# Kernel optimization log

Measured on AMD Instinct MI355X. Metric: run time of the kernel, lower is better.

Reference implementation:

```python
import jax, jax.numpy as jnp
import numpy as np

B, X, S, D_IN, D_OUT = 8, 8, 1024, 512, 64


def setup_inputs() -> dict:
    key = jax.random.key(0)
    ks = jax.random.split(key, 6)
    return {
        "inputs_for_keys": jax.random.normal(ks[0], (B, X, S, D_IN), dtype=jnp.float32),
        "inputs_for_values": jax.random.normal(ks[1], (B, X, S, D_IN), dtype=jnp.float32),
        "inputs_for_queries": jax.random.normal(ks[2], (B, X, S, D_IN), dtype=jnp.float32),
        "k_weight": jax.random.normal(ks[3], (D_IN, D_OUT), dtype=jnp.float32) * (2.0 / (D_IN + D_OUT)) ** 0.5,
        "v_weight": jax.random.normal(ks[4], (D_IN, D_OUT), dtype=jnp.float32) * (2.0 / (D_IN + D_OUT)) ** 0.5,
        "q_weight": jax.random.normal(ks[5], (D_IN, D_OUT), dtype=jnp.float32) * (2.0 / (D_IN + D_OUT)) ** 0.5,
    }


def reference(inputs_for_keys, inputs_for_values, inputs_for_queries, k_weight, v_weight, q_weight):
    # Projections: 'ixjk,kl->ixjl'
    K = jnp.einsum('bxsk,kl->bxsl', inputs_for_keys, k_weight)
    V = jnp.einsum('bxsk,kl->bxsl', inputs_for_values, v_weight)
    Q = jnp.einsum('bxsk,kl->bxsl', inputs_for_queries, q_weight)
    wk = K.shape[2]  # window_size_keys (NOTE: original scales by sqrt(seq_len), not sqrt(d_k))
    scores = jnp.einsum('bxqd,bxkd->bxqk', Q, K) / jnp.sqrt(jnp.float32(wk))
    # causal mask: triu(-inf, k=1) since is_self_attention=True
    causal = jnp.triu(jnp.ones((Q.shape[2], wk), dtype=bool), k=1)  # [Sq, Sk]
    scores = jnp.where(causal[None, None, :, :], -jnp.inf, scores)
    attn = jax.nn.softmax(scores, axis=-1)
    return jnp.einsum('bxqk,bxkd->bxqd', attn, V)
```

## Files before the change

### kernel.cpp

```cpp
#include <hip/hip_runtime.h>
#include <hip/hip_bf16.h>


typedef short  short8 __attribute__((ext_vector_type(8)));
typedef float  f32x4  __attribute__((ext_vector_type(4)));

#define DIN   512
#define DOUT  64
#define SEQ   1024
#define NROWS 65536

__device__ __forceinline__ unsigned short f2bf(float f) {
    unsigned int u = __float_as_uint(f);
    u += 0x7FFF + ((u >> 16) & 1);
    return (unsigned short)(u >> 16);
}

__device__ __forceinline__ unsigned short f2bf_rhu(float f) {
    return (unsigned short)((__float_as_uint(f) + 0x8000u) >> 16);
}

__device__ __forceinline__ float fast_exp2(float x) {
    float r;
    asm("v_exp_f32 %0, %1" : "=v"(r) : "v"(x));
    return r;
}

__global__ __launch_bounds__(256)
void wprep_kernel(const float* __restrict__ k_w, const float* __restrict__ v_w,
                  const float* __restrict__ q_w, unsigned short* __restrict__ Wfrag)
{
    const int mode = blockIdx.y;
    const float* w = (mode == 0) ? k_w : (mode == 1) ? v_w : q_w;
    const float sc = (mode == 2) ? 0.0450842200277801f : 1.0f;
    unsigned short* outp = Wfrag + (size_t)mode * 32768;

    const int s  = blockIdx.x * 256 + threadIdx.x;
    const int l  = s & 63;
    const int nt = (s >> 6) & 3;
    const int kk = s >> 8;
    const int lr = l & 15, lg = l >> 4;
    short8 frag;
    #pragma unroll
    for (int j = 0; j < 8; ++j)
        frag[j] = (short)f2bf(w[(kk * 32 + lg * 8 + j) * 64 + nt * 16 + lr] * sc);
    *(short8*)&outp[(size_t)s * 8] = frag;
}

__global__ __launch_bounds__(512, 2)
void proj_kernel(const float* __restrict__ k_in, const float* __restrict__ v_in,
                 const float* __restrict__ q_in,
                 const unsigned short* __restrict__ Wfrag,
                 unsigned short* __restrict__ Kb, unsigned short* __restrict__ Vf,
                 unsigned short* __restrict__ Qb)
{
    const int mode = blockIdx.y;
    const float* in = (mode == 0) ? k_in : (mode == 1) ? v_in : q_in;
    const unsigned short* wf = Wfrag + (size_t)mode * 32768;

    __shared__ __align__(16) unsigned short Wlds[32768];
    __shared__ __align__(16) unsigned short Alds[2][16384];

    const int tid = threadIdx.x;
    const int wid = tid >> 6;
    const int l   = tid & 63;
    const int lr  = l & 15;
    const int lg  = l >> 4;
    const int r0  = blockIdx.x * 128;

    const int srow = tid >> 5;
    const int scol = tid & 31;
    const float* sbase = in + (size_t)(r0 + srow) * DIN + scol * 4;

    f32x4 rA[8], rB[8];

    #define LOADC(r, c)                                                        \
        { _Pragma("unroll")                                                    \
          for (int i = 0; i < 8; ++i)                                          \
              r[i] = __builtin_nontemporal_load(                               \
                  (const f32x4*)(sbase + (size_t)i * 16 * DIN + (c) * 128)); }

    #define WRITEC(buf, r)                                                     \
        { _Pragma("unroll")                                                    \
          for (int i = 0; i < 8; ++i) {                                        \
              const int row = srow + i * 16;                                   \
              ushort4 pk;                                                      \
              pk.x = f2bf(r[i].x); pk.y = f2bf(r[i].y);                        \
              pk.z = f2bf(r[i].z); pk.w = f2bf(r[i].w);                        \
              *(ushort4*)((char*)&Alds[buf][0] +                               \
                  ((row * 256 + scol * 8) ^ ((row & 7) << 4))) = pk;           \
          } }

    const int arow  = wid * 16 + lr;
    const int abase = arow * 256 + lg * 16;
    const int aswz  = (arow & 7) << 4;

    f32x4 acc[4];
    #pragma unroll
    for (int nt = 0; nt < 4; ++nt)
        #pragma unroll
        for (int i = 0; i < 4; ++i) acc[nt][i] = 0.f;

    #define COMPUTEC(buf, c)                                                   \
        { _Pragma("unroll")                                                    \
          for (int k = 0; k < 4; ++k) {                                        \
              const short8 af = *(const short8*)((const char*)&Alds[buf][0] +  \
                                  ((abase + k * 64) ^ aswz));                  \
              const int kk = (c) * 4 + k;                                      \
              _Pragma("unroll")                                                \
              for (int nt = 0; nt < 4; ++nt) {                                 \
                  const short8 bf = *(const short8*)&Wlds[((kk * 4 + nt) * 64 + l) * 8]; \
                  acc[nt] = __builtin_amdgcn_mfma_f32_16x16x32_bf16(af, bf, acc[nt], 0, 0, 0); \
              }                                                                \
          } }

    LOADC(rA, 0);
    LOADC(rB, 1);
    #pragma unroll
    for (int i = 0; i < 8; ++i)
        *(short8*)&Wlds[(i * 512 + tid) * 8] = *(const short8*)&wf[(size_t)(i * 512 + tid) * 8];
    WRITEC(0, rA);
    __syncthreads();

    LOADC(rA, 2);
    WRITEC(1, rB);
    COMPUTEC(0, 0);
    __syncthreads();
    LOADC(rB, 3);
    WRITEC(0, rA);
    COMPUTEC(1, 1);
    __syncthreads();
    WRITEC(1, rB);
    COMPUTEC(0, 2);
    __syncthreads();
    COMPUTEC(1, 3);

    if (mode == 1) {
        const int grow = r0 + wid * 16 + lg * 4;
        const int bx = grow >> 10;
        const int sl = grow & 1023;
        const int sg = sl >> 5;
        const int lp = (((sl & 31) >> 3) << 4) | lr;
        const int j0 = sl & 7;
        #pragma unroll
        for (int nt = 0; nt < 4; ++nt) {
            ushort4 pk;
            pk.x = f2bf(acc[nt][0]); pk.y = f2bf(acc[nt][1]);
            pk.z = f2bf(acc[nt][2]); pk.w = f2bf(acc[nt][3]);
            *(ushort4*)&Vf[(((size_t)bx * 32 + sg) * 4 + nt) * 512 + (size_t)lp * 8 + j0] = pk;
        }
    } else {
        unsigned short* outp = (mode == 0) ? Kb : Qb;
        const int rbase = r0 + wid * 16 + lg * 4;
        #pragma unroll
        for (int nt = 0; nt < 4; ++nt)
            #pragma unroll
            for (int i = 0; i < 4; ++i)
                outp[(size_t)(rbase + i) * 64 + nt * 16 + lr] = f2bf(acc[nt][i]);
    }
    #undef LOADC
    #undef WRITEC
    #undef COMPUTEC
}

__global__ __launch_bounds__(512)
void attn_kernel(const unsigned short* __restrict__ Qb,
                 const unsigned short* __restrict__ Kb,
                 const unsigned short* __restrict__ Vf,
                 float* __restrict__ out)
{
    __shared__ __align__(16) unsigned short Plds[8][16][72];
    __shared__ __align__(16) f32x4 RedAcc[4][64][4];
    __shared__ float RedSum[4][64][4];

    const int tid  = threadIdx.x;
    const int wid  = tid >> 6;
    const int g    = wid & 3;
    const int half = wid >> 2;
    const int l    = tid & 63;
    const int lr   = l & 15;
    const int lg   = l >> 4;
    const int bx   = blockIdx.x;
    const int qblk = 15 - (int)blockIdx.y;
    const int qw0  = qblk * 64 + g * 16;

    const unsigned short* Qp = Qb + (size_t)bx * 65536;
    const unsigned short* Kp = Kb + (size_t)bx * 65536;
    const unsigned short* Vp = Vf + (size_t)bx * 65536;

    const short8 qa0 = *(const short8*)&Qp[(size_t)(qw0 + lr) * 64 + lg * 8];
    const short8 qa1 = *(const short8*)&Qp[(size_t)(qw0 + lr) * 64 + 32 + lg * 8];

    const int qrow = qw0 + lg * 4;

    float lsum[4] = {0.f, 0.f, 0.f, 0.f};
    f32x4 acc[4];
    #pragma unroll
    for (int dt = 0; dt < 4; ++dt)
        #pragma unroll
        for (int i = 0; i < 4; ++i) acc[dt][i] = 0.f;

    for (int kb = half * 64; kb <= qw0; kb += 128) {
        #pragma unroll
        for (int kt = 0; kt < 4; ++kt) {
            const int kbase = kb + kt * 16;
            if (kbase <= qw0) {
                const short8 k0 = *(const short8*)&Kp[(size_t)(kbase + lr) * 64 + lg * 8];
                const short8 k1 = *(const short8*)&Kp[(size_t)(kbase + lr) * 64 + 32 + lg * 8];
                f32x4 t;
                #pragma unroll
                for (int i = 0; i < 4; ++i) t[i] = 0.f;
                t = __builtin_amdgcn_mfma_f32_16x16x32_bf16(qa0, k0, t, 0, 0, 0);
                t = __builtin_amdgcn_mfma_f32_16x16x32_bf16(qa1, k1, t, 0, 0, 0);
                const int kcol = kbase + lr;
                #pragma unroll
                for (int i = 0; i < 4; ++i) {
                    const float p = (kcol <= qrow + i) ? fast_exp2(t[i] - 8.0f) : 0.f;
                    lsum[i] += p;
                    Plds[wid][lg * 4 + i][kt * 16 + lr] = f2bf_rhu(p);
                }
            } else {
                #pragma unroll
                for (int i = 0; i < 4; ++i)
                    Plds[wid][lg * 4 + i][kt * 16 + lr] = 0;
            }
        }

        asm volatile("s_waitcnt lgkmcnt(0)" ::: "memory");
        __builtin_amdgcn_sched_barrier(0);

        #pragma unroll
        for (int c = 0; c < 2; ++c) {
            if (kb + c * 32 <= qw0 + 15) {
                const short8 pa = *(const short8*)&Plds[wid][lr][c * 32 + lg * 8];
                const size_t vbase = ((size_t)((kb >> 5) + c) * 4) * 512;
                #pragma unroll
                for (int dt = 0; dt < 4; ++dt) {
                    const short8 vbd = *(const short8*)
                        &Vp[vbase + (size_t)dt * 512 + (size_t)l * 8];
                    acc[dt] = __builtin_amdgcn_mfma_f32_16x16x32_bf16(pa, vbd, acc[dt], 0, 0, 0);
                }
            }
        }
        asm volatile("s_waitcnt lgkmcnt(0)" ::: "memory");
    }

    if (half == 1) {
        #pragma unroll
        for (int dt = 0; dt < 4; ++dt) RedAcc[g][l][dt] = acc[dt];
        #pragma unroll
        for (int i = 0; i < 4; ++i) RedSum[g][l][i] = lsum[i];
    }
    __syncthreads();
    if (half == 0) {
        #pragma unroll
        for (int dt = 0; dt < 4; ++dt) acc[dt] += RedAcc[g][l][dt];
        #pragma unroll
        for (int i = 0; i < 4; ++i) lsum[i] += RedSum[g][l][i];

        #pragma unroll
        for (int d = 1; d < 16; d <<= 1)
            #pragma unroll
            for (int i = 0; i < 4; ++i) lsum[i] += __shfl_xor(lsum[i], d);

        float inv[4];
        #pragma unroll
        for (int i = 0; i < 4; ++i) inv[i] = 1.0f / lsum[i];

        const size_t orow = (size_t)bx * 1024 + qw0;
        #pragma unroll
        for (int dt = 0; dt < 4; ++dt)
            #pragma unroll
            for (int i = 0; i < 4; ++i)
                out[(orow + lg * 4 + i) * 64 + dt * 16 + lr] = acc[dt][i] * inv[i];
    }
}

extern "C" void kernel_launch(void* const* d_in, const int* in_sizes, int n_in,
                              void* d_out, int out_size, void* d_ws, size_t ws_size,
                              hipStream_t stream) {
    const float* k_in = (const float*)d_in[0];
    const float* v_in = (const float*)d_in[1];
    const float* q_in = (const float*)d_in[2];
    const float* k_w  = (const float*)d_in[3];
    const float* v_w  = (const float*)d_in[4];
    const float* q_w  = (const float*)d_in[5];

    unsigned short* Kb    = (unsigned short*)d_ws;
    unsigned short* Vf    = Kb + (size_t)NROWS * 64;
    unsigned short* Qb    = Vf + (size_t)NROWS * 64;
    unsigned short* Wfrag = Qb + (size_t)NROWS * 64;

    wprep_kernel<<<dim3(16, 3), 256, 0, stream>>>(k_w, v_w, q_w, Wfrag);
    proj_kernel<<<dim3(512, 3), 512, 0, stream>>>(
        k_in, v_in, q_in, Wfrag, Kb, Vf, Qb);
    attn_kernel<<<dim3(64, 16), 512, 0, stream>>>(Qb, Kb, Vf, (float*)d_out);
}
```

Baseline: 132.9 us.

## Make projection A-tile staging wave-private to drop block barriers

Each wave now loads, converts and stores its own 16 input rows into a private LDS region. It then consumes those rows in its own MFMAs, so the per-chunk __syncthreads between write and compute are removed and only one barrier remains, after the weight load. This is meant to remove barrier stalls and let waves run their load/convert/compute pipeline independently. Global loads now cover 2 rows per wave-instruction instead of 16 rows per block, and correctness relies on wave-level ordering of LDS writes and reads without explicit barriers.

```diff
diff --git a/kernel.cpp b/kernel.cpp
--- a/kernel.cpp
+++ b/kernel.cpp
@@ -59,18 +59,18 @@
     const unsigned short* wf = Wfrag + (size_t)mode * 32768;
 
     __shared__ __align__(16) unsigned short Wlds[32768];
-    __shared__ __align__(16) unsigned short Alds[2][16384];
+    __shared__ __align__(16) unsigned short Alds[8][2][2048];
 
     const int tid = threadIdx.x;
     const int wid = tid >> 6;
     const int l   = tid & 63;
     const int lr  = l & 15;
     const int lg  = l >> 4;
-    const int r0  = blockIdx.x * 128;
-
-    const int srow = tid >> 5;
-    const int scol = tid & 31;
-    const float* sbase = in + (size_t)(r0 + srow) * DIN + scol * 4;
+    const int r0  = blockIdx.x * 128 + wid * 16;
+
+    const int srow = l >> 5;
+    const int scolb = (l & 31) * 8;
+    const float* sbase = in + (size_t)(r0 + srow) * DIN + (l & 31) * 4;
 
     f32x4 rA[8], rB[8];
 
@@ -78,22 +78,21 @@
         { _Pragma("unroll")                                                    \
           for (int i = 0; i < 8; ++i)                                          \
               r[i] = __builtin_nontemporal_load(                               \
-                  (const f32x4*)(sbase + (size_t)i * 16 * DIN + (c) * 128)); }
+                  (const f32x4*)(sbase + (size_t)(2 * i) * DIN + (c) * 128)); }
 
     #define WRITEC(buf, r)                                                     \
         { _Pragma("unroll")                                                    \
           for (int i = 0; i < 8; ++i) {                                        \
-              const int row = srow + i * 16;                                   \
+              const int row = 2 * i + srow;                                    \
               ushort4 pk;                                                      \
               pk.x = f2bf(r[i].x); pk.y = f2bf(r[i].y);                        \
               pk.z = f2bf(r[i].z); pk.w = f2bf(r[i].w);                        \
-              *(ushort4*)((char*)&Alds[buf][0] +                               \
-                  ((row * 256 + scol * 8) ^ ((row & 7) << 4))) = pk;           \
+              *(ushort4*)((char*)&Alds[wid][buf][0] +                          \
+                  ((row * 256 + scolb) ^ ((row & 7) << 4))) = pk;              \
           } }
 
-    const int arow  = wid * 16 + lr;
-    const int abase = arow * 256 + lg * 16;
-    const int aswz  = (arow & 7) << 4;
+    const int abase = lr * 256 + lg * 16;
+    const int aswz  = (lr & 7) << 4;
 
     f32x4 acc[4];
     #pragma unroll
@@ -104,7 +103,7 @@
     #define COMPUTEC(buf, c)                                                   \
         { _Pragma("unroll")                                                    \
           for (int k = 0; k < 4; ++k) {                                        \
-              const short8 af = *(const short8*)((const char*)&Alds[buf][0] +  \
+              const short8 af = *(const short8*)((const char*)&Alds[wid][buf][0] + \
                                   ((abase + k * 64) ^ aswz));                  \
               const int kk = (c) * 4 + k;                                      \
               _Pragma("unroll")                                                \
@@ -119,24 +118,24 @@
     #pragma unroll
     for (int i = 0; i < 8; ++i)
         *(short8*)&Wlds[(i * 512 + tid) * 8] = *(const short8*)&wf[(size_t)(i * 512 + tid) * 8];
+    __syncthreads();
+
     WRITEC(0, rA);
-    __syncthreads();
-
     LOADC(rA, 2);
+    COMPUTEC(0, 0);
+
     WRITEC(1, rB);
-    COMPUTEC(0, 0);
-    __syncthreads();
     LOADC(rB, 3);
+    COMPUTEC(1, 1);
+
     WRITEC(0, rA);
-    COMPUTEC(1, 1);
-    __syncthreads();
+    COMPUTEC(0, 2);
+
     WRITEC(1, rB);
-    COMPUTEC(0, 2);
-    __syncthreads();
     COMPUTEC(1, 3);
 
     if (mode == 1) {
-        const int grow = r0 + wid * 16 + lg * 4;
+        const int grow = r0 + lg * 4;
         const int bx = grow >> 10;
         const int sl = grow & 1023;
         const int sg = sl >> 5;
@@ -151,7 +150,7 @@
         }
     } else {
         unsigned short* outp = (mode == 0) ? Kb : Qb;
-        const int rbase = r0 + wid * 16 + lg * 4;
+        const int rbase = r0 + lg * 4;
         #pragma unroll
         for (int nt = 0; nt < 4; ++nt)
             #pragma unroll
```

After: 128.5 us. -3.3%, faster.
